# Kernel optimization log

Measured on AMD Instinct MI355X. Metric: run time of the kernel, lower is better.

Reference implementation:

```python
import jax, jax.numpy as jnp
import numpy as np

# ---- config ----
N = 500000
C = 32            # output_coordinate_dim
RES = [256, 256, 256, 64]
J = 2             # wavelet levels
BOUNDS = 1.3
# plane i -> (H, W) of stored plane, and (q, r) coord indices into [x,y,z,t]
# grid_sample convention: coord0 indexes W, coord1 indexes H
PLANE_RES = [(256, 256), (256, 256), (256, 64), (256, 256), (256, 64), (256, 64)]
COORD_IDX = [(0, 1), (0, 2), (3, 0), (1, 2), (3, 1), (3, 2)]

# coif4 decomposition low-pass filter (pywt), 24 taps
DEC_LO = np.array([
    -1.7849850030882614e-06, -3.2596802368833675e-06, 3.1229875865345646e-05,
    6.233903446100713e-05, -0.00025997455248771324, -0.0005890207562443383,
    0.0012665619292989445, 0.003751436157278457, -0.00565828668661072,
    -0.015211731527946259, 0.025082261844864097, 0.03933442712333749,
    -0.09622044203398798, -0.06662747426342504, 0.4343860564914685,
    0.782238930920499, 0.41530840703043026, -0.05607731331675481,
    -0.08126669968087875, 0.026682300156053072, 0.016068943964776348,
    -0.0073461663276420935, -0.0016294920126017326, 0.0008923136685823146],
    dtype=np.float32)
REC_LO = DEC_LO[::-1].copy()                                    # synthesis low-pass
REC_HI = (DEC_LO * ((-1.0) ** np.arange(DEC_LO.shape[0]))).astype(np.float32)  # QMF high-pass


def _up2(x, axis):
    """Insert zeros between samples along axis (upsample by 2)."""
    x = jnp.moveaxis(x, axis, -1)
    z = jnp.zeros(x.shape[:-1] + (2 * x.shape[-1],), x.dtype)
    z = z.at[..., ::2].set(x)
    return jnp.moveaxis(z, -1, axis)


def _circ_conv(x, f, axis):
    """Circular convolution along axis with a short fixed filter (periodization mode)."""
    out = f[0] * x
    for k in range(1, len(f)):
        out = out + f[k] * jnp.roll(x, k, axis=axis)
    return out


def _sfb1d(lo, hi, axis):
    """1D synthesis filter bank: upsample, filter, add. Length L -> 2L."""
    return _circ_conv(_up2(lo, axis), REC_LO, axis) + _circ_conv(_up2(hi, axis), REC_HI, axis)


def _sfb_level(ll, yh):
    """One inverse-DWT level. ll: [1,C,h,w], yh: [1,C,3,h,w] -> [1,C,2h,2w]."""
    lh, hl, hh = yh[:, :, 0], yh[:, :, 1], yh[:, :, 2]
    lo = _sfb1d(ll, lh, axis=2)   # combine along H
    hi = _sfb1d(hl, hh, axis=2)
    return _sfb1d(lo, hi, axis=3)  # combine along W


def _idwt2(yl, yhb, yha):
    """2-level inverse DWT (coif4, periodization). yl coarsest, yhb coarse detail, yha fine detail."""
    x = _sfb_level(yl, yhb)   # H/4 -> H/2
    x = _sfb_level(x, yha)    # H/2 -> H
    return x                  # [1, C, H, W]


def _bilinear_sample(plane, coords):
    """torch.grid_sample(bilinear, align_corners=True) equivalent.
    plane: [C,H,W]; coords: [N,2] in [-1,1], coords[:,0]->W, coords[:,1]->H. Returns [N,C]."""
    Cc, H, W = plane.shape
    x = jnp.clip((coords[:, 0] + 1.0) * 0.5 * (W - 1), 0.0, W - 1.0)
    y = jnp.clip((coords[:, 1] + 1.0) * 0.5 * (H - 1), 0.0, H - 1.0)
    x0 = jnp.clip(jnp.floor(x), 0.0, W - 2.0)
    y0 = jnp.clip(jnp.floor(y), 0.0, H - 2.0)
    wx = x - x0
    wy = y - y0
    x0i = x0.astype(jnp.int32); x1i = x0i + 1
    y0i = y0.astype(jnp.int32); y1i = y0i + 1
    v = (plane[:, y0i, x0i] * (1 - wy) * (1 - wx)
         + plane[:, y0i, x1i] * (1 - wy) * wx
         + plane[:, y1i, x0i] * wy * (1 - wx)
         + plane[:, y1i, x1i] * wy * wx)  # [C,N]
    return v.T


def setup_inputs() -> dict:
    key = jax.random.key(0)
    keys = jax.random.split(key, 2 + 6 * 3)
    inp = {}
    inp["pts"] = jax.random.uniform(keys[0], (N, 3), jnp.float32, -BOUNDS, BOUNDS)
    inp["timestamps"] = jax.random.uniform(keys[1], (N, 1), jnp.float32, 0.0, 1.0)
    for i, (H, W) in enumerate(PLANE_RES):
        k0, k1, k2 = keys[2 + 3 * i], keys[2 + 3 * i + 1], keys[2 + 3 * i + 2]
        # wavelet-domain learned parameters: yl coarsest approx, yha fine detail, yhb coarse detail
        inp[f"yl{i}"] = 0.3 + 0.1 * jax.random.normal(k0, (1, C, H // 4, W // 4), jnp.float32)
        inp[f"yha{i}"] = 0.05 * jax.random.normal(k1, (1, C, 3, H // 2, W // 2), jnp.float32)
        inp[f"yhb{i}"] = 0.05 * jax.random.normal(k2, (1, C, 3, H // 4, W // 4), jnp.float32)
    return inp


def reference(pts, timestamps,
              yl0, yha0, yhb0, yl1, yha1, yhb1, yl2, yha2, yhb2,
              yl3, yha3, yhb3, yl4, yha4, yhb4, yl5, yha5, yhb5):
    coefs = [(yl0, yha0, yhb0), (yl1, yha1, yhb1), (yl2, yha2, yhb2),
             (yl3, yha3, yhb3), (yl4, yha4, yhb4), (yl5, yha5, yhb5)]
    # normalize_aabb with aabb = [[B,B,B],[-B,-B,-B]]
    pts_n = (pts - BOUNDS) * (2.0 / (-2.0 * BOUNDS)) - 1.0
    t = timestamps * 2.0 - 1.0
    p4 = jnp.concatenate([pts_n, t], axis=-1)  # [N,4] = (x,y,z,t) in [-1,1]
    interp = jnp.ones((), jnp.float32)
    for (yl, yha, yhb), (q, r) in zip(coefs, COORD_IDX):
        plane = _idwt2(yl, yhb, yha)[0]                      # [C,H,W] IDWT reconstruction
        coords = jnp.stack([p4[:, q], p4[:, r]], axis=-1)    # [N,2]
        feat = _bilinear_sample(plane, coords)               # [N,C] gather
        interp = interp * feat                               # multiplicative fusion
    return interp
```

## Files before the change

kernel.cpp:

```cpp
#include <hip/hip_runtime.h>
#include <hip/hip_fp16.h>

#define NBIN 4096
#define CAP 256
#define OVCAP 65536

__device__ __constant__ float DEC_LO[24] = {
    -1.7849850030882614e-06f, -3.2596802368833675e-06f, 3.1229875865345646e-05f,
    6.233903446100713e-05f, -0.00025997455248771324f, -0.0005890207562443383f,
    0.0012665619292989445f, 0.003751436157278457f, -0.00565828668661072f,
    -0.015211731527946259f, 0.025082261844864097f, 0.03933442712333749f,
    -0.09622044203398798f, -0.06662747426342504f, 0.4343860564914685f,
    0.782238930920499f, 0.41530840703043026f, -0.05607731331675481f,
    -0.08126669968087875f, 0.026682300156053072f, 0.016068943964776348f,
    -0.0073461663276420935f, -0.0016294920126017326f, 0.0008923136685823146f
};

struct PK {
    const float* yl[6];
    const float* yhb[6];
    const float* yha[6];
    float* x1[6];
    __half* lo2[6];
    __half* hi2[6];
    __half* planeH[6];
    const float* pts;
    const float* ts;
    int* cnt;
    float4* binP4;
    int* binIdx;
    float4* ovP4;
    int* ovIdx;
    int Npts;
};

__device__ __forceinline__ void compute_p4(const float* pts, const float* ts, int p, float* p4) {
    const float sc = (float)(2.0 / (-2.0 * 1.3));
    p4[0] = (pts[p * 3 + 0] - 1.3f) * sc - 1.0f;
    p4[1] = (pts[p * 3 + 1] - 1.3f) * sc - 1.0f;
    p4[2] = (pts[p * 3 + 2] - 1.3f) * sc - 1.0f;
    p4[3] = ts[p] * 2.0f - 1.0f;
}

__device__ __forceinline__ int morton_key(const float* p4) {
    int key = 0;
#pragma unroll
    for (int d = 0; d < 4; ++d) {
        float u = (p4[d] + 1.0f) * 0.5f * 8.0f;
        int ci = (int)u;
        ci = ci < 0 ? 0 : (ci > 7 ? 7 : ci);
#pragma unroll
        for (int b = 0; b < 3; ++b) key |= ((ci >> b) & 1) << (b * 4 + d);
    }
    return key;
}

__global__ __launch_bounds__(256) void k1_l1_zero(PK a) {
    __shared__ struct { float lo[32 * 64], hi[32 * 64]; } sm;
    int bid = blockIdx.x, tid = threadIdx.x;

    if (bid < 768) {
        int rg = bid & 3, c = (bid >> 2) & 31, i = bid >> 7;
        int w4 = (i == 0 || i == 1 || i == 3) ? 64 : 16;
        int lw4 = (w4 == 64) ? 6 : 4;

        const float* llc = a.yl[i] + (size_t)c * 64 * w4;
        const float* lhc = a.yhb[i] + (size_t)(c * 3 + 0) * 64 * w4;
        const float* hlc = a.yhb[i] + (size_t)(c * 3 + 1) * 64 * w4;
        const float* hhc = a.yhb[i] + (size_t)(c * 3 + 2) * 64 * w4;

        for (int idx = tid; idx < (16 << lw4); idx += 256) {
            int mp = idx >> lw4, x = idx & (w4 - 1);
            int m = rg * 16 + mp;
            float lo0 = 0.f, lo1 = 0.f, hi0 = 0.f, hi1 = 0.f;
#pragma unroll
            for (int j = 0; j < 12; ++j) {
                int r = (m - j) & 63;
                int ii = (r << lw4) + x;
                float vll = llc[ii], vlh = lhc[ii], vhl = hlc[ii], vhh = hhc[ii];
                float rl0 = DEC_LO[23 - 2 * j], rl1 = DEC_LO[22 - 2 * j];
                float rh0 = DEC_LO[2 * j],      rh1 = -DEC_LO[2 * j + 1];
                lo0 += rl0 * vll + rh0 * vlh;
                lo1 += rl1 * vll + rh1 * vlh;
                hi0 += rl0 * vhl + rh0 * vhh;
                hi1 += rl1 * vhl + rh1 * vhh;
            }
            sm.lo[((2 * mp) << lw4) + x] = lo0;
            sm.lo[((2 * mp + 1) << lw4) + x] = lo1;
            sm.hi[((2 * mp) << lw4) + x] = hi0;
            sm.hi[((2 * mp + 1) << lw4) + x] = hi1;
        }
        __syncthreads();

        int w2 = w4 * 2;
        float* x1p = a.x1[i] + (size_t)c * 128 * w2;
        for (int idx = tid; idx < (32 << lw4); idx += 256) {
            int yl = idx >> lw4, mcol = idx & (w4 - 1);
            float o0 = 0.f, o1 = 0.f;
#pragma unroll
            for (int j = 0; j < 12; ++j) {
                int r = (mcol - j) & (w4 - 1);
                float vl = sm.lo[(yl << lw4) + r], vh = sm.hi[(yl << lw4) + r];
                o0 += DEC_LO[23 - 2 * j] * vl + DEC_LO[2 * j] * vh;
                o1 += DEC_LO[22 - 2 * j] * vl - DEC_LO[2 * j + 1] * vh;
            }
            *(float2*)(x1p + (size_t)(rg * 32 + yl) * w2 + 2 * mcol) = make_float2(o0, o1);
        }
    } else {
        int idx = (bid - 768) * 256 + tid;
        if (idx <= NBIN) a.cnt[idx] = 0;
    }
}

__global__ __launch_bounds__(256) void k2_v2_scatter(PK a) {
    int bid = blockIdx.x, tid = threadIdx.x;

    if (bid < 7680) {
        const int boff[7] = {0, 2048, 4096, 4608, 6656, 7168, 7680};
        int i = 0;
        while (i < 5 && bid >= boff[i + 1]) ++i;
        int lw2 = (i == 0 || i == 1 || i == 3) ? 7 : 5;
        int w2 = 1 << lw2;
        unsigned t = (unsigned)(bid - boff[i]) * 256u + tid;
        unsigned hw = 128u << lw2;
        unsigned c = t >> (7 + lw2);
        unsigned rem = t & (hw - 1);
        unsigned m = rem >> lw2;
        unsigned x = rem & (unsigned)(w2 - 1);

        const float* llc = a.x1[i] + (size_t)c * hw;
        const float* lhc = a.yha[i] + (size_t)(c * 3 + 0) * hw;
        const float* hlc = a.yha[i] + (size_t)(c * 3 + 1) * hw;
        const float* hhc = a.yha[i] + (size_t)(c * 3 + 2) * hw;

        float lo0 = 0.f, lo1 = 0.f, hi0 = 0.f, hi1 = 0.f;
#pragma unroll
        for (int j = 0; j < 12; ++j) {
            int r = ((int)m - j) & 127;
            unsigned idx = ((unsigned)r << lw2) + x;
            float vll = llc[idx], vlh = lhc[idx], vhl = hlc[idx], vhh = hhc[idx];
            float rl0 = DEC_LO[23 - 2 * j], rl1 = DEC_LO[22 - 2 * j];
            float rh0 = DEC_LO[2 * j],      rh1 = -DEC_LO[2 * j + 1];
            lo0 += rl0 * vll + rh0 * vlh;
            lo1 += rl1 * vll + rh1 * vlh;
            hi0 += rl0 * vhl + rh0 * vhh;
            hi1 += rl1 * vhl + rh1 * vhh;
        }
        size_t ob = ((size_t)c * 256 + 2 * m) * w2 + x;
        a.lo2[i][ob] = __float2half(lo0);
        a.lo2[i][ob + w2] = __float2half(lo1);
        a.hi2[i][ob] = __float2half(hi0);
        a.hi2[i][ob + w2] = __float2half(hi1);
    } else {
        for (int p = (bid - 7680) * 256 + tid; p < a.Npts; p += 512 * 256) {
            float p4[4];
            compute_p4(a.pts, a.ts, p, p4);
            int key = morton_key(p4);
            int pos = atomicAdd(&a.cnt[key], 1);
            if (pos < CAP) {
                a.binP4[key * CAP + pos] = make_float4(p4[0], p4[1], p4[2], p4[3]);
                a.binIdx[key * CAP + pos] = p;
            } else {
                int ov = atomicAdd(&a.cnt[NBIN], 1);
                if (ov < OVCAP) {
                    a.ovP4[ov] = make_float4(p4[0], p4[1], p4[2], p4[3]);
                    a.ovIdx[ov] = p;
                }
            }
        }
    }
}

__global__ __launch_bounds__(256) void k3_ht(PK a) {
    __shared__ struct { __half lo[32 * 130], hi[32 * 130]; } sm;
    int bid = blockIdx.x, tid = threadIdx.x;
    int i = bid >> 8, y = bid & 255;
    int lw2 = (i == 0 || i == 1 || i == 3) ? 7 : 5;
    int w2 = 1 << lw2;
    int stride = w2 + 2;

    for (int idx = tid; idx < (32 << lw2); idx += 256) {
        int c = idx >> lw2, x = idx & (w2 - 1);
        size_t g = ((size_t)c * 256 + y) * w2 + x;
        sm.lo[c * stride + x] = a.lo2[i][g];
        sm.hi[c * stride + x] = a.hi2[i][g];
    }
    __syncthreads();

    int W = 2 * w2;
    __half* orow = a.planeH[i] + (size_t)y * W * 32;
    for (int idx = tid; idx < (32 << lw2); idx += 256) {
        int m = idx >> 5, c = idx & 31;
        float o0 = 0.f, o1 = 0.f;
#pragma unroll
        for (int j = 0; j < 12; ++j) {
            int r2 = m - j; if (r2 < 0) r2 += w2;
            float vl = __half2float(sm.lo[c * stride + r2]);
            float vh = __half2float(sm.hi[c * stride + r2]);
            o0 += DEC_LO[23 - 2 * j] * vl + DEC_LO[2 * j] * vh;
            o1 += DEC_LO[22 - 2 * j] * vl - DEC_LO[2 * j + 1] * vh;
        }
        orow[(2 * m) * 32 + c] = __float2half(o0);
        orow[(2 * m + 1) * 32 + c] = __float2half(o1);
    }
}

union H8 { float4 f4; __half h[8]; };

struct SK {
    const __half* pl[6];
    const float4* binP4;
    const int* binIdx;
    const int* cnt;
    const float4* ovP4;
    const int* ovIdx;
    float* out;
};

__device__ __forceinline__ void sample_point(const SK& a, const float* p4, int oidx, int ch8) {
    const int PW[6] = {256, 256, 64, 256, 64, 64};
    const int QI[6] = {0, 0, 3, 1, 3, 3};
    const int RI[6] = {1, 2, 0, 2, 1, 2};
    float acc[8] = {1.f, 1.f, 1.f, 1.f, 1.f, 1.f, 1.f, 1.f};
#pragma unroll
    for (int i = 0; i < 6; ++i) {
        int W = PW[i];
        float cx = p4[QI[i]];
        float cy = p4[RI[i]];
        float fx = (cx + 1.0f) * 0.5f * (float)(W - 1);
        fx = fminf(fmaxf(fx, 0.0f), (float)(W - 1));
        float fy = (cy + 1.0f) * 0.5f * 255.0f;
        fy = fminf(fmaxf(fy, 0.0f), 255.0f);
        float x0 = fminf(fmaxf(floorf(fx), 0.0f), (float)(W - 2));
        float y0 = fminf(fmaxf(floorf(fy), 0.0f), 254.0f);
        float wx = fx - x0, wy = fy - y0;
        int xi = (int)x0, yi = (int)y0;

        const __half* base = a.pl[i] + ((size_t)yi * W + xi) * 32 + ch8;
        H8 u00, u01, u10, u11;
        u00.f4 = *(const float4*)(base);
        u01.f4 = *(const float4*)(base + 32);
        u10.f4 = *(const float4*)(base + (size_t)W * 32);
        u11.f4 = *(const float4*)(base + (size_t)W * 32 + 32);

        float w00 = (1.f - wy) * (1.f - wx), w01 = (1.f - wy) * wx;
        float w10 = wy * (1.f - wx), w11 = wy * wx;
#pragma unroll
        for (int k = 0; k < 8; ++k) {
            float f = w00 * __half2float(u00.h[k]) + w01 * __half2float(u01.h[k]) +
                      w10 * __half2float(u10.h[k]) + w11 * __half2float(u11.h[k]);
            acc[k] *= f;
        }
    }
    float* op = a.out + (size_t)oidx * 32 + ch8;
    *(float4*)(op) = make_float4(acc[0], acc[1], acc[2], acc[3]);
    *(float4*)(op + 4) = make_float4(acc[4], acc[5], acc[6], acc[7]);
}

__global__ __launch_bounds__(256) void k4_sample(SK a) {
    int bid = blockIdx.x, tid = threadIdx.x;
    if (bid < NBIN) {
        int bin = (bid & 7) * (NBIN / 8) + (bid >> 3);
        int n = a.cnt[bin];
        n = n < CAP ? n : CAP;
        const float4* bp = a.binP4 + bin * CAP;
        const int* bi = a.binIdx + bin * CAP;
        for (int l = tid; l < n * 4; l += 256) {
            int s = l >> 2, ch8 = (l & 3) << 3;
            float4 q = bp[s];
            float p4[4] = {q.x, q.y, q.z, q.w};
            sample_point(a, p4, bi[s], ch8);
        }
    } else {
        int ov = a.cnt[NBIN];
        ov = ov < OVCAP ? ov : OVCAP;
        for (int l = (bid - NBIN) * 256 + tid; l < ov * 4; l += 8 * 256) {
            int s = l >> 2, ch8 = (l & 3) << 3;
            float4 q = a.ovP4[s];
            float p4[4] = {q.x, q.y, q.z, q.w};
            sample_point(a, p4, a.ovIdx[s], ch8);
        }
    }
}

extern "C" void kernel_launch(void* const* d_in, const int* in_sizes, int n_in,
                              void* d_out, int out_size, void* d_ws, size_t ws_size,
                              hipStream_t stream) {
    const int PWt[6] = {256, 256, 64, 256, 64, 64};
    const int Npts = in_sizes[0] / 3;

    char* ws = (char*)d_ws;
    PK a;
    size_t off = 0;
    for (int i = 0; i < 6; ++i) {
        int W = PWt[i], w2 = W / 2;
        a.x1[i] = (float*)(ws + off);      off += (size_t)32 * 128 * w2 * 4;
        a.lo2[i] = (__half*)(ws + off);    off += (size_t)32 * 256 * w2 * 2;
        a.hi2[i] = (__half*)(ws + off);    off += (size_t)32 * 256 * w2 * 2;
        a.planeH[i] = (__half*)(ws + off); off += (size_t)256 * W * 32 * 2;
    }
    off = (off + 15) & ~(size_t)15;
    a.binP4 = (float4*)(ws + off);  off += (size_t)NBIN * CAP * 16;
    a.ovP4 = (float4*)(ws + off);   off += (size_t)OVCAP * 16;
    a.binIdx = (int*)(ws + off);    off += (size_t)NBIN * CAP * 4;
    a.ovIdx = (int*)(ws + off);     off += (size_t)OVCAP * 4;
    a.cnt = (int*)(ws + off);       off += (NBIN + 1) * 4;

    a.pts = (const float*)d_in[0];
    a.ts = (const float*)d_in[1];
    for (int i = 0; i < 6; ++i) {
        a.yl[i] = (const float*)d_in[2 + 3 * i];
        a.yha[i] = (const float*)d_in[3 + 3 * i];
        a.yhb[i] = (const float*)d_in[4 + 3 * i];
    }
    a.Npts = Npts;

    k1_l1_zero<<<768 + 17, 256, 0, stream>>>(a);
    k2_v2_scatter<<<7680 + 512, 256, 0, stream>>>(a);
    k3_ht<<<1536, 256, 0, stream>>>(a);

    SK s;
    for (int i = 0; i < 6; ++i) s.pl[i] = a.planeH[i];
    s.binP4 = a.binP4; s.binIdx = a.binIdx; s.cnt = a.cnt;
    s.ovP4 = a.ovP4; s.ovIdx = a.ovIdx;
    s.out = (float*)d_out;
    k4_sample<<<NBIN + 8, 256, 0, stream>>>(s);
}
```

Measured before the change: 274.3 us.

## Schedule scatter blocks first, batch atomics, and interleave plane-filter block order

The point-binning blocks now take the low block indices, so they are dispatched first and overlap with the vertical synthesis filter blocks instead of trailing behind them. Each scatter thread processes four points per iteration and issues their atomics together, giving more memory-level parallelism. The filter blocks are remapped in an interleaved order so different planes run concurrently. In exchange there is extra index arithmetic, and the atomic and scatter work may contend with the filter blocks for bandwidth.

```diff
diff --git a/kernel.cpp b/kernel.cpp
--- a/kernel.cpp
+++ b/kernel.cpp
@@ -115,13 +115,53 @@
 __global__ __launch_bounds__(256) void k2_v2_scatter(PK a) {
     int bid = blockIdx.x, tid = threadIdx.x;
 
-    if (bid < 7680) {
+    if (bid < 512) {
+        const int S = 512 * 256;
+        int t = bid * 256 + tid;
+        for (int base = 0; base < a.Npts; base += 4 * S) {
+            float4 q[4];
+            int key[4], pi[4], pos[4];
+#pragma unroll
+            for (int k = 0; k < 4; ++k) {
+                int p = base + t + k * S;
+                pi[k] = p;
+                if (p < a.Npts) {
+                    float p4[4];
+                    compute_p4(a.pts, a.ts, p, p4);
+                    key[k] = morton_key(p4);
+                    q[k] = make_float4(p4[0], p4[1], p4[2], p4[3]);
+                } else {
+                    key[k] = -1;
+                }
+            }
+#pragma unroll
+            for (int k = 0; k < 4; ++k)
+                if (key[k] >= 0) pos[k] = atomicAdd(&a.cnt[key[k]], 1);
+#pragma unroll
+            for (int k = 0; k < 4; ++k) {
+                if (key[k] < 0) continue;
+                if (pos[k] < CAP) {
+                    a.binP4[key[k] * CAP + pos[k]] = q[k];
+                    a.binIdx[key[k] * CAP + pos[k]] = pi[k];
+                } else {
+                    int ov = atomicAdd(&a.cnt[NBIN], 1);
+                    if (ov < OVCAP) {
+                        a.ovP4[ov] = q[k];
+                        a.ovIdx[ov] = pi[k];
+                    }
+                }
+            }
+        }
+    } else {
+        int ib = bid - 512;
+        ib = (ib & 7) * 960 + (ib >> 3);
+
         const int boff[7] = {0, 2048, 4096, 4608, 6656, 7168, 7680};
         int i = 0;
-        while (i < 5 && bid >= boff[i + 1]) ++i;
+        while (i < 5 && ib >= boff[i + 1]) ++i;
         int lw2 = (i == 0 || i == 1 || i == 3) ? 7 : 5;
         int w2 = 1 << lw2;
-        unsigned t = (unsigned)(bid - boff[i]) * 256u + tid;
+        unsigned t = (unsigned)(ib - boff[i]) * 256u + tid;
         unsigned hw = 128u << lw2;
         unsigned c = t >> (7 + lw2);
         unsigned rem = t & (hw - 1);
@@ -151,23 +191,6 @@
         a.lo2[i][ob + w2] = __float2half(lo1);
         a.hi2[i][ob] = __float2half(hi0);
         a.hi2[i][ob + w2] = __float2half(hi1);
-    } else {
-        for (int p = (bid - 7680) * 256 + tid; p < a.Npts; p += 512 * 256) {
-            float p4[4];
-            compute_p4(a.pts, a.ts, p, p4);
-            int key = morton_key(p4);
-            int pos = atomicAdd(&a.cnt[key], 1);
-            if (pos < CAP) {
-                a.binP4[key * CAP + pos] = make_float4(p4[0], p4[1], p4[2], p4[3]);
-                a.binIdx[key * CAP + pos] = p;
-            } else {
-                int ov = atomicAdd(&a.cnt[NBIN], 1);
-                if (ov < OVCAP) {
-                    a.ovP4[ov] = make_float4(p4[0], p4[1], p4[2], p4[3]);
-                    a.ovIdx[ov] = p;
-                }
-            }
-        }
     }
 }
 
@@ -316,7 +339,7 @@
     a.Npts = Npts;
 
     k1_l1_zero<<<768 + 17, 256, 0, stream>>>(a);
-    k2_v2_scatter<<<7680 + 512, 256, 0, stream>>>(a);
+    k2_v2_scatter<<<512 + 7680, 256, 0, stream>>>(a);
     k3_ht<<<1536, 256, 0, stream>>>(a);
 
     SK s;
```

Measured after the change: 272.5 us. About the same (-0.7%).

## Drop Morton binning of points and vectorize level-two vertical synthesis

Applied to the files above, without the earlier changes.

Removes the spatial binning pass, which used atomic counters to scatter points into Morton-ordered bins. The sampler now walks points directly in input order, computing normalized coordinates inline. Separately, the second-level vertical synthesis now handles four columns per thread, using float4 loads and packed half2 stores, with an interleaved block index. This drops the scatter and atomic cost and the extra workspace traffic, at the risk of less gather locality across the planes during sampling.

```diff
diff --git a/kernel.cpp b/kernel.cpp
--- a/kernel.cpp
+++ b/kernel.cpp
@@ -1,9 +1,5 @@
 #include <hip/hip_runtime.h>
 #include <hip/hip_fp16.h>
-
-#define NBIN 4096
-#define CAP 256
-#define OVCAP 65536
 
 __device__ __constant__ float DEC_LO[24] = {
     -1.7849850030882614e-06f, -3.2596802368833675e-06f, 3.1229875865345646e-05f,
@@ -24,121 +20,30 @@
     __half* lo2[6];
     __half* hi2[6];
     __half* planeH[6];
-    const float* pts;
-    const float* ts;
-    int* cnt;
-    float4* binP4;
-    int* binIdx;
-    float4* ovP4;
-    int* ovIdx;
-    int Npts;
 };
 
-__device__ __forceinline__ void compute_p4(const float* pts, const float* ts, int p, float* p4) {
-    const float sc = (float)(2.0 / (-2.0 * 1.3));
-    p4[0] = (pts[p * 3 + 0] - 1.3f) * sc - 1.0f;
-    p4[1] = (pts[p * 3 + 1] - 1.3f) * sc - 1.0f;
-    p4[2] = (pts[p * 3 + 2] - 1.3f) * sc - 1.0f;
-    p4[3] = ts[p] * 2.0f - 1.0f;
-}
-
-__device__ __forceinline__ int morton_key(const float* p4) {
-    int key = 0;
-#pragma unroll
-    for (int d = 0; d < 4; ++d) {
-        float u = (p4[d] + 1.0f) * 0.5f * 8.0f;
-        int ci = (int)u;
-        ci = ci < 0 ? 0 : (ci > 7 ? 7 : ci);
-#pragma unroll
-        for (int b = 0; b < 3; ++b) key |= ((ci >> b) & 1) << (b * 4 + d);
-    }
-    return key;
-}
-
-__global__ __launch_bounds__(256) void k1_l1_zero(PK a) {
+__global__ __launch_bounds__(256) void k1_l1(PK a) {
     __shared__ struct { float lo[32 * 64], hi[32 * 64]; } sm;
     int bid = blockIdx.x, tid = threadIdx.x;
 
-    if (bid < 768) {
-        int rg = bid & 3, c = (bid >> 2) & 31, i = bid >> 7;
-        int w4 = (i == 0 || i == 1 || i == 3) ? 64 : 16;
-        int lw4 = (w4 == 64) ? 6 : 4;
-
-        const float* llc = a.yl[i] + (size_t)c * 64 * w4;
-        const float* lhc = a.yhb[i] + (size_t)(c * 3 + 0) * 64 * w4;
-        const float* hlc = a.yhb[i] + (size_t)(c * 3 + 1) * 64 * w4;
-        const float* hhc = a.yhb[i] + (size_t)(c * 3 + 2) * 64 * w4;
-
-        for (int idx = tid; idx < (16 << lw4); idx += 256) {
-            int mp = idx >> lw4, x = idx & (w4 - 1);
-            int m = rg * 16 + mp;
-            float lo0 = 0.f, lo1 = 0.f, hi0 = 0.f, hi1 = 0.f;
-#pragma unroll
-            for (int j = 0; j < 12; ++j) {
-                int r = (m - j) & 63;
-                int ii = (r << lw4) + x;
-                float vll = llc[ii], vlh = lhc[ii], vhl = hlc[ii], vhh = hhc[ii];
-                float rl0 = DEC_LO[23 - 2 * j], rl1 = DEC_LO[22 - 2 * j];
-                float rh0 = DEC_LO[2 * j],      rh1 = -DEC_LO[2 * j + 1];
-                lo0 += rl0 * vll + rh0 * vlh;
-                lo1 += rl1 * vll + rh1 * vlh;
-                hi0 += rl0 * vhl + rh0 * vhh;
-                hi1 += rl1 * vhl + rh1 * vhh;
-            }
-            sm.lo[((2 * mp) << lw4) + x] = lo0;
-            sm.lo[((2 * mp + 1) << lw4) + x] = lo1;
-            sm.hi[((2 * mp) << lw4) + x] = hi0;
-            sm.hi[((2 * mp + 1) << lw4) + x] = hi1;
-        }
-        __syncthreads();
-
-        int w2 = w4 * 2;
-        float* x1p = a.x1[i] + (size_t)c * 128 * w2;
-        for (int idx = tid; idx < (32 << lw4); idx += 256) {
-            int yl = idx >> lw4, mcol = idx & (w4 - 1);
-            float o0 = 0.f, o1 = 0.f;
-#pragma unroll
-            for (int j = 0; j < 12; ++j) {
-                int r = (mcol - j) & (w4 - 1);
-                float vl = sm.lo[(yl << lw4) + r], vh = sm.hi[(yl << lw4) + r];
-                o0 += DEC_LO[23 - 2 * j] * vl + DEC_LO[2 * j] * vh;
-                o1 += DEC_LO[22 - 2 * j] * vl - DEC_LO[2 * j + 1] * vh;
-            }
-            *(float2*)(x1p + (size_t)(rg * 32 + yl) * w2 + 2 * mcol) = make_float2(o0, o1);
-        }
-    } else {
-        int idx = (bid - 768) * 256 + tid;
-        if (idx <= NBIN) a.cnt[idx] = 0;
-    }
-}
-
-__global__ __launch_bounds__(256) void k2_v2_scatter(PK a) {
-    int bid = blockIdx.x, tid = threadIdx.x;
-
-    if (bid < 7680) {
-        const int boff[7] = {0, 2048, 4096, 4608, 6656, 7168, 7680};
-        int i = 0;
-        while (i < 5 && bid >= boff[i + 1]) ++i;
-        int lw2 = (i == 0 || i == 1 || i == 3) ? 7 : 5;
-        int w2 = 1 << lw2;
-        unsigned t = (unsigned)(bid - boff[i]) * 256u + tid;
-        unsigned hw = 128u << lw2;
-        unsigned c = t >> (7 + lw2);
-        unsigned rem = t & (hw - 1);
-        unsigned m = rem >> lw2;
-        unsigned x = rem & (unsigned)(w2 - 1);
-
-        const float* llc = a.x1[i] + (size_t)c * hw;
-        const float* lhc = a.yha[i] + (size_t)(c * 3 + 0) * hw;
-        const float* hlc = a.yha[i] + (size_t)(c * 3 + 1) * hw;
-        const float* hhc = a.yha[i] + (size_t)(c * 3 + 2) * hw;
-
+    int rg = bid & 3, c = (bid >> 2) & 31, i = bid >> 7;
+    int w4 = (i == 0 || i == 1 || i == 3) ? 64 : 16;
+    int lw4 = (w4 == 64) ? 6 : 4;
+
+    const float* llc = a.yl[i] + (size_t)c * 64 * w4;
+    const float* lhc = a.yhb[i] + (size_t)(c * 3 + 0) * 64 * w4;
+    const float* hlc = a.yhb[i] + (size_t)(c * 3 + 1) * 64 * w4;
+    const float* hhc = a.yhb[i] + (size_t)(c * 3 + 2) * 64 * w4;
+
+    for (int idx = tid; idx < (16 << lw4); idx += 256) {
+        int mp = idx >> lw4, x = idx & (w4 - 1);
+        int m = rg * 16 + mp;
         float lo0 = 0.f, lo1 = 0.f, hi0 = 0.f, hi1 = 0.f;
 #pragma unroll
         for (int j = 0; j < 12; ++j) {
-            int r = ((int)m - j) & 127;
-            unsigned idx = ((unsigned)r << lw2) + x;
-            float vll = llc[idx], vlh = lhc[idx], vhl = hlc[idx], vhh = hhc[idx];
+            int r = (m - j) & 63;
+            int ii = (r << lw4) + x;
+            float vll = llc[ii], vlh = lhc[ii], vhl = hlc[ii], vhh = hhc[ii];
             float rl0 = DEC_LO[23 - 2 * j], rl1 = DEC_LO[22 - 2 * j];
             float rh0 = DEC_LO[2 * j],      rh1 = -DEC_LO[2 * j + 1];
             lo0 += rl0 * vll + rh0 * vlh;
@@ -146,34 +51,88 @@
             hi0 += rl0 * vhl + rh0 * vhh;
             hi1 += rl1 * vhl + rh1 * vhh;
         }
-        size_t ob = ((size_t)c * 256 + 2 * m) * w2 + x;
-        a.lo2[i][ob] = __float2half(lo0);
-        a.lo2[i][ob + w2] = __float2half(lo1);
-        a.hi2[i][ob] = __float2half(hi0);
-        a.hi2[i][ob + w2] = __float2half(hi1);
-    } else {
-        for (int p = (bid - 7680) * 256 + tid; p < a.Npts; p += 512 * 256) {
-            float p4[4];
-            compute_p4(a.pts, a.ts, p, p4);
-            int key = morton_key(p4);
-            int pos = atomicAdd(&a.cnt[key], 1);
-            if (pos < CAP) {
-                a.binP4[key * CAP + pos] = make_float4(p4[0], p4[1], p4[2], p4[3]);
-                a.binIdx[key * CAP + pos] = p;
-            } else {
-                int ov = atomicAdd(&a.cnt[NBIN], 1);
-                if (ov < OVCAP) {
-                    a.ovP4[ov] = make_float4(p4[0], p4[1], p4[2], p4[3]);
-                    a.ovIdx[ov] = p;
-                }
-            }
-        }
-    }
+        sm.lo[((2 * mp) << lw4) + x] = lo0;
+        sm.lo[((2 * mp + 1) << lw4) + x] = lo1;
+        sm.hi[((2 * mp) << lw4) + x] = hi0;
+        sm.hi[((2 * mp + 1) << lw4) + x] = hi1;
+    }
+    __syncthreads();
+
+    int w2 = w4 * 2;
+    float* x1p = a.x1[i] + (size_t)c * 128 * w2;
+    for (int idx = tid; idx < (32 << lw4); idx += 256) {
+        int yl = idx >> lw4, mcol = idx & (w4 - 1);
+        float o0 = 0.f, o1 = 0.f;
+#pragma unroll
+        for (int j = 0; j < 12; ++j) {
+            int r = (mcol - j) & (w4 - 1);
+            float vl = sm.lo[(yl << lw4) + r], vh = sm.hi[(yl << lw4) + r];
+            o0 += DEC_LO[23 - 2 * j] * vl + DEC_LO[2 * j] * vh;
+            o1 += DEC_LO[22 - 2 * j] * vl - DEC_LO[2 * j + 1] * vh;
+        }
+        *(float2*)(x1p + (size_t)(rg * 32 + yl) * w2 + 2 * mcol) = make_float2(o0, o1);
+    }
+}
+
+__global__ __launch_bounds__(256) void k2_v2(PK a) {
+    int ib = blockIdx.x, tid = threadIdx.x;
+    ib = (ib & 7) * 240 + (ib >> 3);
+
+    const int boff[7] = {0, 512, 1024, 1152, 1664, 1792, 1920};
+    int i = 0;
+    while (i < 5 && ib >= boff[i + 1]) ++i;
+    int lw2 = (i == 0 || i == 1 || i == 3) ? 7 : 5;
+    int w2 = 1 << lw2;
+    unsigned t = (unsigned)(ib - boff[i]) * 256u + tid;
+    unsigned tpc = 32u << lw2;
+    unsigned c = t >> (5 + lw2);
+    unsigned rem = t & (tpc - 1);
+    unsigned m = rem >> (lw2 - 2);
+    unsigned x = (rem & (unsigned)((w2 >> 2) - 1)) * 4;
+    unsigned hw = 128u << lw2;
+
+    const float* llc = a.x1[i] + (size_t)c * hw;
+    const float* lhc = a.yha[i] + (size_t)(c * 3 + 0) * hw;
+    const float* hlc = a.yha[i] + (size_t)(c * 3 + 1) * hw;
+    const float* hhc = a.yha[i] + (size_t)(c * 3 + 2) * hw;
+
+    float4 acl0 = {0,0,0,0}, acl1 = {0,0,0,0}, ach0 = {0,0,0,0}, ach1 = {0,0,0,0};
+#pragma unroll
+    for (int j = 0; j < 12; ++j) {
+        int r = ((int)m - j) & 127;
+        unsigned idx = ((unsigned)r << lw2) + x;
+        float4 vll = *(const float4*)(llc + idx);
+        float4 vlh = *(const float4*)(lhc + idx);
+        float4 vhl = *(const float4*)(hlc + idx);
+        float4 vhh = *(const float4*)(hhc + idx);
+        float rl0 = DEC_LO[23 - 2 * j], rl1 = DEC_LO[22 - 2 * j];
+        float rh0 = DEC_LO[2 * j],      rh1 = -DEC_LO[2 * j + 1];
+        acl0.x += rl0 * vll.x + rh0 * vlh.x;  acl0.y += rl0 * vll.y + rh0 * vlh.y;
+        acl0.z += rl0 * vll.z + rh0 * vlh.z;  acl0.w += rl0 * vll.w + rh0 * vlh.w;
+        acl1.x += rl1 * vll.x + rh1 * vlh.x;  acl1.y += rl1 * vll.y + rh1 * vlh.y;
+        acl1.z += rl1 * vll.z + rh1 * vlh.z;  acl1.w += rl1 * vll.w + rh1 * vlh.w;
+        ach0.x += rl0 * vhl.x + rh0 * vhh.x;  ach0.y += rl0 * vhl.y + rh0 * vhh.y;
+        ach0.z += rl0 * vhl.z + rh0 * vhh.z;  ach0.w += rl0 * vhl.w + rh0 * vhh.w;
+        ach1.x += rl1 * vhl.x + rh1 * vhh.x;  ach1.y += rl1 * vhl.y + rh1 * vhh.y;
+        ach1.z += rl1 * vhl.z + rh1 * vhh.z;  ach1.w += rl1 * vhl.w + rh1 * vhh.w;
+    }
+    size_t ob = ((size_t)c * 256 + 2 * m) * w2 + x;
+    __half* lp = a.lo2[i] + ob;
+    *(__half2*)(lp)          = __floats2half2_rn(acl0.x, acl0.y);
+    *(__half2*)(lp + 2)      = __floats2half2_rn(acl0.z, acl0.w);
+    *(__half2*)(lp + w2)     = __floats2half2_rn(acl1.x, acl1.y);
+    *(__half2*)(lp + w2 + 2) = __floats2half2_rn(acl1.z, acl1.w);
+    __half* hpp = a.hi2[i] + ob;
+    *(__half2*)(hpp)          = __floats2half2_rn(ach0.x, ach0.y);
+    *(__half2*)(hpp + 2)      = __floats2half2_rn(ach0.z, ach0.w);
+    *(__half2*)(hpp + w2)     = __floats2half2_rn(ach1.x, ach1.y);
+    *(__half2*)(hpp + w2 + 2) = __floats2half2_rn(ach1.z, ach1.w);
 }
 
 __global__ __launch_bounds__(256) void k3_ht(PK a) {
     __shared__ struct { __half lo[32 * 130], hi[32 * 130]; } sm;
     int bid = blockIdx.x, tid = threadIdx.x;
+
     int i = bid >> 8, y = bid & 255;
     int lw2 = (i == 0 || i == 1 || i == 3) ? 7 : 5;
     int w2 = 1 << lw2;
@@ -209,12 +168,10 @@
 
 struct SK {
     const __half* pl[6];
-    const float4* binP4;
-    const int* binIdx;
-    const int* cnt;
-    const float4* ovP4;
-    const int* ovIdx;
+    const float* pts;
+    const float* ts;
     float* out;
+    int Npts;
 };
 
 __device__ __forceinline__ void sample_point(const SK& a, const float* p4, int oidx, int ch8) {
@@ -225,14 +182,10 @@
 #pragma unroll
     for (int i = 0; i < 6; ++i) {
         int W = PW[i];
-        float cx = p4[QI[i]];
-        float cy = p4[RI[i]];
-        float fx = (cx + 1.0f) * 0.5f * (float)(W - 1);
-        fx = fminf(fmaxf(fx, 0.0f), (float)(W - 1));
-        float fy = (cy + 1.0f) * 0.5f * 255.0f;
-        fy = fminf(fmaxf(fy, 0.0f), 255.0f);
-        float x0 = fminf(fmaxf(floorf(fx), 0.0f), (float)(W - 2));
-        float y0 = fminf(fmaxf(floorf(fy), 0.0f), 254.0f);
+        float fx = fminf(fmaxf((p4[QI[i]] + 1.0f) * 0.5f * (float)(W - 1), 0.0f), (float)(W - 1));
+        float fy = fminf(fmaxf((p4[RI[i]] + 1.0f) * 0.5f * 255.0f, 0.0f), 255.0f);
+        float x0 = fminf(floorf(fx), (float)(W - 2));
+        float y0 = fminf(floorf(fy), 254.0f);
         float wx = fx - x0, wy = fy - y0;
         int xi = (int)x0, yi = (int)y0;
 
@@ -257,29 +210,18 @@
     *(float4*)(op + 4) = make_float4(acc[4], acc[5], acc[6], acc[7]);
 }
 
-__global__ __launch_bounds__(256) void k4_sample(SK a) {
-    int bid = blockIdx.x, tid = threadIdx.x;
-    if (bid < NBIN) {
-        int bin = (bid & 7) * (NBIN / 8) + (bid >> 3);
-        int n = a.cnt[bin];
-        n = n < CAP ? n : CAP;
-        const float4* bp = a.binP4 + bin * CAP;
-        const int* bi = a.binIdx + bin * CAP;
-        for (int l = tid; l < n * 4; l += 256) {
-            int s = l >> 2, ch8 = (l & 3) << 3;
-            float4 q = bp[s];
-            float p4[4] = {q.x, q.y, q.z, q.w};
-            sample_point(a, p4, bi[s], ch8);
-        }
-    } else {
-        int ov = a.cnt[NBIN];
-        ov = ov < OVCAP ? ov : OVCAP;
-        for (int l = (bid - NBIN) * 256 + tid; l < ov * 4; l += 8 * 256) {
-            int s = l >> 2, ch8 = (l & 3) << 3;
-            float4 q = a.ovP4[s];
-            float p4[4] = {q.x, q.y, q.z, q.w};
-            sample_point(a, p4, a.ovIdx[s], ch8);
-        }
+__global__ __launch_bounds__(256) void k4_direct(SK a) {
+    const float sc = (float)(2.0 / (-2.0 * 1.3));
+    int n4 = a.Npts * 4;
+    int gs = gridDim.x * 256;
+    for (int l = blockIdx.x * 256 + threadIdx.x; l < n4; l += gs) {
+        int s = l >> 2, ch8 = (l & 3) << 3;
+        float p4[4];
+        p4[0] = (a.pts[s * 3 + 0] - 1.3f) * sc - 1.0f;
+        p4[1] = (a.pts[s * 3 + 1] - 1.3f) * sc - 1.0f;
+        p4[2] = (a.pts[s * 3 + 2] - 1.3f) * sc - 1.0f;
+        p4[3] = a.ts[s] * 2.0f - 1.0f;
+        sample_point(a, p4, s, ch8);
     }
 }
 
@@ -292,37 +234,31 @@
     char* ws = (char*)d_ws;
     PK a;
     size_t off = 0;
+    __half* planes[6];
     for (int i = 0; i < 6; ++i) {
         int W = PWt[i], w2 = W / 2;
         a.x1[i] = (float*)(ws + off);      off += (size_t)32 * 128 * w2 * 4;
         a.lo2[i] = (__half*)(ws + off);    off += (size_t)32 * 256 * w2 * 2;
         a.hi2[i] = (__half*)(ws + off);    off += (size_t)32 * 256 * w2 * 2;
         a.planeH[i] = (__half*)(ws + off); off += (size_t)256 * W * 32 * 2;
-    }
-    off = (off + 15) & ~(size_t)15;
-    a.binP4 = (float4*)(ws + off);  off += (size_t)NBIN * CAP * 16;
-    a.ovP4 = (float4*)(ws + off);   off += (size_t)OVCAP * 16;
-    a.binIdx = (int*)(ws + off);    off += (size_t)NBIN * CAP * 4;
-    a.ovIdx = (int*)(ws + off);     off += (size_t)OVCAP * 4;
-    a.cnt = (int*)(ws + off);       off += (NBIN + 1) * 4;
-
-    a.pts = (const float*)d_in[0];
-    a.ts = (const float*)d_in[1];
+        planes[i] = a.planeH[i];
+    }
+
     for (int i = 0; i < 6; ++i) {
         a.yl[i] = (const float*)d_in[2 + 3 * i];
         a.yha[i] = (const float*)d_in[3 + 3 * i];
         a.yhb[i] = (const float*)d_in[4 + 3 * i];
     }
-    a.Npts = Npts;
-
-    k1_l1_zero<<<768 + 17, 256, 0, stream>>>(a);
-    k2_v2_scatter<<<7680 + 512, 256, 0, stream>>>(a);
+
+    k1_l1<<<768, 256, 0, stream>>>(a);
+    k2_v2<<<1920, 256, 0, stream>>>(a);
     k3_ht<<<1536, 256, 0, stream>>>(a);
 
     SK s;
-    for (int i = 0; i < 6; ++i) s.pl[i] = a.planeH[i];
-    s.binP4 = a.binP4; s.binIdx = a.binIdx; s.cnt = a.cnt;
-    s.ovP4 = a.ovP4; s.ovIdx = a.ovIdx;
+    for (int i = 0; i < 6; ++i) s.pl[i] = planes[i];
+    s.pts = (const float*)d_in[0];
+    s.ts = (const float*)d_in[1];
     s.out = (float*)d_out;
-    k4_sample<<<NBIN + 8, 256, 0, stream>>>(s);
-}
+    s.Npts = Npts;
+    k4_direct<<<4096, 256, 0, stream>>>(s);
+}
```

Result: faster. 267.4 us (-2.5%).
